# Kernel optimization log

Hardware: AMD Instinct MI355X
Metric: run time of the kernel (lower is better)

The kernel has to match this reference:

```python
import jax, jax.numpy as jnp
import numpy as np

N = 50000      # nodes
E = 800000     # edges (avg degree 16)
D_IN = 32      # raw feature dim
D = 96         # hidden == out dim (residual requires equality)
L = 4          # number of GatedGCN layers
NC = 10        # n_classes
EPS = 1e-6


def _w(k, shape, fan_in):
    return jax.random.normal(k, shape, jnp.float32) / np.sqrt(fan_in).astype(np.float32)


def setup_inputs() -> dict:
    key = jax.random.key(0)
    ks = jax.random.split(key, 16)
    inp = {
        'h': jax.random.normal(ks[0], (N, D_IN), jnp.float32),
        'e': jax.random.normal(ks[1], (E, D_IN), jnp.float32),
        'src': jax.random.randint(ks[2], (E,), 0, N, jnp.int32),
        'dst': jax.random.randint(ks[3], (E,), 0, N, jnp.int32),
        'fp_w': _w(ks[4], (D_IN, D), D_IN), 'fp_b': jnp.zeros((D,), jnp.float32),
        'ep_w': _w(ks[5], (D_IN, D), D_IN), 'ep_b': jnp.zeros((D,), jnp.float32),
    }
    for i, name in enumerate(['A', 'B', 'C', 'D', 'E']):
        inp[name + '_w'] = _w(ks[6 + i], (L, D, D), D)
        inp[name + '_b'] = jnp.zeros((L, D), jnp.float32)
    inp['mlp0_w'] = _w(ks[11], (D, D // 2), D); inp['mlp0_b'] = jnp.zeros((D // 2,), jnp.float32)
    inp['mlp1_w'] = _w(ks[12], (D // 2, D // 4), D // 2); inp['mlp1_b'] = jnp.zeros((D // 4,), jnp.float32)
    inp['mlp2_w'] = _w(ks[13], (D // 4, NC), D // 4); inp['mlp2_b'] = jnp.zeros((NC,), jnp.float32)
    return inp


def reference(h, e, src, dst, fp_w, fp_b, ep_w, ep_b,
              A_w, A_b, B_w, B_b, C_w, C_b, D_w, D_b, E_w, E_b,
              mlp0_w, mlp0_b, mlp1_w, mlp1_b, mlp2_w, mlp2_b):
    # input projections
    h = h @ fp_w + fp_b                       # [N, D]
    e = e @ ep_w + ep_b                       # [E, D]

    def layer(carry, p):
        h, e = carry
        Aw, Ab, Bw, Bb, Cw, Cb, Dw, Db, Ew, Eb = p
        Ah = h @ Aw + Ab
        Bh = h @ Bw + Bb
        Ce = e @ Cw + Cb
        Dh = h @ Dw + Db
        Eh = h @ Ew + Eb
        # edge gate: e_ij = D h_i + E h_j + C e_ij  (u_add_v with u=src, v=dst)
        e_new = Dh[src] + Eh[dst] + Ce          # [E, D]
        sigma = jax.nn.sigmoid(e_new)           # [E, D]
        # gated aggregation to destination nodes
        num = jax.ops.segment_sum(Bh[src] * sigma, dst, num_segments=N)  # [N, D]
        den = jax.ops.segment_sum(sigma, dst, num_segments=N)            # [N, D]
        h_new = Ah + num / (den + EPS)
        # relu then residual (batch_norm=False, dropout eval no-op)
        return (h + jax.nn.relu(h_new), e + jax.nn.relu(e_new)), None

    (h, e), _ = jax.lax.scan(layer, (h, e),
                             (A_w, A_b, B_w, B_b, C_w, C_b, D_w, D_b, E_w, E_b))

    # MLPReadout (L=2 halvings) + sigmoid head
    y = jax.nn.relu(h @ mlp0_w + mlp0_b)
    y = jax.nn.relu(y @ mlp1_w + mlp1_b)
    y = y @ mlp2_w + mlp2_b
    return jax.nn.sigmoid(y)                    # [N, NC]
```

## Files before the change

### kernel.cpp

```cpp
#include <hip/hip_runtime.h>

#define NN 50000
#define NE 800000
#define DIN 32
#define DD 96
#define NL 4
#define NCLS 10
#define EPSF 1e-6f

typedef unsigned short u16;
typedef unsigned int u32;

typedef __bf16 bf16x8 __attribute__((ext_vector_type(8)));
typedef float f32x4 __attribute__((ext_vector_type(4)));

static __device__ __forceinline__ u16 f2bf(float f) {
    u32 x = __float_as_uint(f);
    x += 0x7FFFu + ((x >> 16) & 1u);
    return (u16)(x >> 16);
}
static __device__ __forceinline__ u32 pk2(float a, float b) {
    u32 r;
    asm("v_cvt_pk_bf16_f32 %0, %1, %2" : "=v"(r) : "v"(a), "v"(b));
    return r;
}
static __device__ __forceinline__ float unlo(u32 u) { return __uint_as_float(u << 16); }
static __device__ __forceinline__ float unhi(u32 u) { return __uint_as_float(u & 0xFFFF0000u); }
static __device__ __forceinline__ float frcp(float x) { return __builtin_amdgcn_rcpf(x); }

__global__ void k_zero4(int* __restrict__ p, long n4) {
    long i = (long)blockIdx.x * blockDim.x + threadIdx.x;
    if (i < n4) ((int4*)p)[i] = make_int4(0, 0, 0, 0);
}

__global__ void k_hist(const int* __restrict__ dst, int* __restrict__ counts) {
    int i = blockIdx.x * blockDim.x + threadIdx.x;
    if (i < NE) atomicAdd(&counts[dst[i]], 1);
}

__global__ __launch_bounds__(1024) void k_scan1(const int* __restrict__ counts,
                                                int* __restrict__ excl,
                                                int* __restrict__ bsum, int n) {
    __shared__ int wsum[16];
    const int tid = threadIdx.x, lane = tid & 63, wid = tid >> 6;
    const int i = blockIdx.x * 1024 + tid;
    int v = (i < n) ? counts[i] : 0;
    int x = v;
#pragma unroll
    for (int off = 1; off < 64; off <<= 1) {
        int t = __shfl_up(x, (unsigned)off, 64);
        if (lane >= off) x += t;
    }
    if (lane == 63) wsum[wid] = x;
    __syncthreads();
    if (tid < 16) {
        int s = wsum[tid];
#pragma unroll
        for (int off = 1; off < 16; off <<= 1) {
            int t = __shfl_up(s, (unsigned)off, 16);
            if (tid >= off) s += t;
        }
        wsum[tid] = s;
    }
    __syncthreads();
    const int wbase = wid ? wsum[wid - 1] : 0;
    if (i < n) excl[i] = wbase + x - v;
    if (tid == 1023) bsum[blockIdx.x] = wbase + x;
}

__global__ void k_scan2(int* __restrict__ bsum, int nb) {
    const int lane = threadIdx.x;
    int v = (lane < nb) ? bsum[lane] : 0;
    int x = v;
#pragma unroll
    for (int off = 1; off < 64; off <<= 1) {
        int t = __shfl_up(x, (unsigned)off, 64);
        if (lane >= off) x += t;
    }
    if (lane < nb) bsum[lane] = x - v;
}

__global__ void k_scan3(int* __restrict__ row_ptr, int* __restrict__ cursor,
                        const int* __restrict__ bsum, int n) {
    int i = blockIdx.x * blockDim.x + threadIdx.x;
    if (i < n) {
        int v = row_ptr[i] + bsum[i >> 10];
        row_ptr[i] = v;
        cursor[i] = v;
    }
    if (i == 0) row_ptr[n] = NE;
}

__global__ void k_scatter(const int* __restrict__ src, const int* __restrict__ dst,
                          int* __restrict__ cursor, int* __restrict__ eperm,
                          int* __restrict__ srcp) {
    int i = blockIdx.x * blockDim.x + threadIdx.x;
    if (i >= NE) return;
    int pos = atomicAdd(&cursor[dst[i]], 1);
    eperm[pos] = i;
    srcp[pos] = src[i];
}

__global__ void k_packAll(const float* __restrict__ A_w, const float* __restrict__ B_w,
                          const float* __restrict__ C_w, const float* __restrict__ D_w,
                          const float* __restrict__ E_w,
                          const float* __restrict__ fp_w, const float* __restrict__ ep_w,
                          const float* __restrict__ m0w,
                          u16* __restrict__ awf, u16* __restrict__ bwf, u16* __restrict__ cwf,
                          u16* __restrict__ dwf, u16* __restrict__ ewf,
                          u16* __restrict__ wfp, u16* __restrict__ wep,
                          float* __restrict__ w0p) {
    const int PER = NL * 6 * 3 * 64;
    int q = blockIdx.x * blockDim.x + threadIdx.x;
    if (q < 5 * PER) {
        int which = q / PER;
        int qq = q - which * PER;
        const float* W_all = which == 0 ? A_w : which == 1 ? B_w : which == 2 ? C_w
                           : which == 3 ? D_w : E_w;
        u16* wf = which == 0 ? awf : which == 1 ? bwf : which == 2 ? cwf
                : which == 3 ? dwf : ewf;
        int l = qq / (6 * 3 * 64);
        int rem = qq - l * (6 * 3 * 64);
        int tile = rem / (3 * 64);
        int rem2 = rem - tile * (3 * 64);
        int c = rem2 >> 6, ln = rem2 & 63;
        const float* W = W_all + (long)l * DD * DD;
        int n = tile * 16 + (ln & 15);
        int k0 = c * 32 + (ln >> 4) * 8;
        u16 wv[8];
#pragma unroll
        for (int j = 0; j < 8; ++j) {
            int kk = k0 + j;
            int kact = (kk % 6) * 16 + kk / 6;
            wv[j] = f2bf(W[kact * DD + n]);
        }
        *(uint4*)&wf[(long)qq * 8] = *(uint4*)wv;
    } else if (q < 5 * PER + 768) {
        int qq = q - 5 * PER;
        int which = qq / 384; qq -= which * 384;
        const float* W = which ? ep_w : fp_w;
        u16* wf = which ? wep : wfp;
        int ln = qq & 63;
        int n = (qq >> 6) * 16 + (ln & 15);
        int k0 = (ln >> 4) * 8;
        u16 wv[8];
#pragma unroll
        for (int j = 0; j < 8; ++j) wv[j] = f2bf(W[(k0 + j) * DD + n]);
        *(uint4*)&wf[qq * 8] = *(uint4*)wv;
    } else {
        int qq = q - 5 * PER - 768;
        if (qq < DD * 48) {
            int p = qq / 48, j = qq - p * 48;
            int jp = (p % 6) * 16 + p / 6;
            w0p[qq] = m0w[jp * 48 + j];
        }
    }
}

template <bool BFOUT, bool PERM, bool POUT>
__global__ __launch_bounds__(256) void k_proj_m(const float* __restrict__ X,
                                                const u16* __restrict__ wf,
                                                const float* __restrict__ B,
                                                void* __restrict__ Y,
                                                const int* __restrict__ eperm,
                                                int ntiles) {
    const int lane = threadIdx.x & 63;
    const int gw = (blockIdx.x * blockDim.x + threadIdx.x) >> 6;
    const int nw = (gridDim.x * blockDim.x) >> 6;
    const int lm = lane & 15, quad = lane >> 4;

    bf16x8 bfr[6];
    float bias[6];
#pragma unroll
    for (int t = 0; t < 6; ++t) {
        bfr[t] = *(const bf16x8*)&wf[(t * 64 + lane) * 8];
        bias[t] = B[t * 16 + lm];
    }

    for (int tile = gw; tile < ntiles; tile += nw) {
        const int row = tile * 16 + lm;
        const long srow = PERM ? (long)eperm[row] : (long)row;
        float4 x0 = *(const float4*)&X[srow * DIN + quad * 8];
        float4 x1 = *(const float4*)&X[srow * DIN + quad * 8 + 4];
        u32 ap[4] = {pk2(x0.x, x0.y), pk2(x0.z, x0.w), pk2(x1.x, x1.y), pk2(x1.z, x1.w)};
        bf16x8 af = *(bf16x8*)ap;
        f32x4 acc[6];
#pragma unroll
        for (int t = 0; t < 6; ++t) {
            acc[t] = (f32x4){bias[t], bias[t], bias[t], bias[t]};
            acc[t] = __builtin_amdgcn_mfma_f32_16x16x32_bf16(af, bfr[t], acc[t], 0, 0, 0);
        }
        const long rbase = (long)tile * 16 + quad * 4;
        if (POUT) {
#pragma unroll
            for (int r = 0; r < 4; ++r) {
                if (BFOUT) {
                    u16* p = (u16*)Y + (rbase + r) * DD + lm * 6;
                    *(u32*)p       = pk2(acc[0][r], acc[1][r]);
                    *(u32*)(p + 2) = pk2(acc[2][r], acc[3][r]);
                    *(u32*)(p + 4) = pk2(acc[4][r], acc[5][r]);
                } else {
                    float* p = (float*)Y + (rbase + r) * DD + lm * 6;
                    *(float2*)(p)     = make_float2(acc[0][r], acc[1][r]);
                    *(float2*)(p + 2) = make_float2(acc[2][r], acc[3][r]);
                    *(float2*)(p + 4) = make_float2(acc[4][r], acc[5][r]);
                }
            }
        } else {
#pragma unroll
            for (int t = 0; t < 6; ++t) {
                const int j = t * 16 + lm;
#pragma unroll
                for (int r = 0; r < 4; ++r) {
                    float v = acc[t][r];
                    if (BFOUT) ((u16*)Y)[(rbase + r) * DD + j] = f2bf(v);
                    else       ((float*)Y)[(rbase + r) * DD + j] = v;
                }
            }
        }
    }
}

__global__ __launch_bounds__(256) void k_gemm4m(const float* __restrict__ X,
                                                const u16* __restrict__ awf, const float* __restrict__ ab,
                                                const u16* __restrict__ bwf, const float* __restrict__ bb,
                                                const u16* __restrict__ dwf, const float* __restrict__ db,
                                                const u16* __restrict__ ewf, const float* __restrict__ eb,
                                                float* __restrict__ Y0, u16* __restrict__ Y1,
                                                u16* __restrict__ Y2, u16* __restrict__ Y3,
                                                int ntiles) {
    const int lane = threadIdx.x & 63;
    const int w = threadIdx.x >> 6;
    const int lm = lane & 15, quad = lane >> 4;
    const u16* wf = (w == 0) ? awf : (w == 1) ? bwf : (w == 2) ? dwf : ewf;
    const float* bp = (w == 0) ? ab : (w == 1) ? bb : (w == 2) ? db : eb;

    bf16x8 bfr[6][3];
    float bias[6];
#pragma unroll
    for (int t = 0; t < 6; ++t) {
#pragma unroll
        for (int c = 0; c < 3; ++c)
            bfr[t][c] = *(const bf16x8*)&wf[((t * 3 + c) * 64 + lane) * 8];
        bias[t] = bp[t * 16 + lm];
    }

    for (int tile = blockIdx.x; tile < ntiles; tile += gridDim.x) {
        const float* xr = X + (long)(tile * 16 + lm) * DD;
        bf16x8 a[3];
#pragma unroll
        for (int c = 0; c < 3; ++c) {
            float4 x0 = *(const float4*)&xr[c * 32 + quad * 8];
            float4 x1 = *(const float4*)&xr[c * 32 + quad * 8 + 4];
            u32 ap[4] = {pk2(x0.x, x0.y), pk2(x0.z, x0.w), pk2(x1.x, x1.y), pk2(x1.z, x1.w)};
            a[c] = *(bf16x8*)ap;
        }
        f32x4 acc[6];
#pragma unroll
        for (int t = 0; t < 6; ++t) {
            acc[t] = (f32x4){bias[t], bias[t], bias[t], bias[t]};
#pragma unroll
            for (int c = 0; c < 3; ++c)
                acc[t] = __builtin_amdgcn_mfma_f32_16x16x32_bf16(a[c], bfr[t][c], acc[t], 0, 0, 0);
        }
        const long rbase = (long)tile * 16 + quad * 4;
        if (w == 0) {
#pragma unroll
            for (int r = 0; r < 4; ++r) {
                float* p = Y0 + (rbase + r) * DD + lm * 6;
                *(float2*)(p)     = make_float2(acc[0][r], acc[1][r]);
                *(float2*)(p + 2) = make_float2(acc[2][r], acc[3][r]);
                *(float2*)(p + 4) = make_float2(acc[4][r], acc[5][r]);
            }
        } else {
            u16* Yp = (w == 1) ? Y1 : (w == 2) ? Y2 : Y3;
#pragma unroll
            for (int r = 0; r < 4; ++r) {
                u16* p = Yp + (rbase + r) * DD + lm * 6;
                *(u32*)p       = pk2(acc[0][r], acc[1][r]);
                *(u32*)(p + 2) = pk2(acc[2][r], acc[3][r]);
                *(u32*)(p + 4) = pk2(acc[4][r], acc[5][r]);
            }
        }
    }
}

__global__ __launch_bounds__(256) void k_node_edge_w(u16* ebuf,
                                                     const u16* __restrict__ cwf,
                                                     const float* __restrict__ Cb,
                                                     const u16* __restrict__ Dh,
                                                     const u16* __restrict__ Eh,
                                                     const u16* __restrict__ Bh,
                                                     const int* __restrict__ srcp,
                                                     const int* __restrict__ row_ptr,
                                                     const float* __restrict__ Ah,
                                                     float* __restrict__ hbuf) {
    const int lane = threadIdx.x & 63;
    const int gw = (blockIdx.x * blockDim.x + threadIdx.x) >> 6;
    const int nw = (gridDim.x * blockDim.x) >> 6;
    const int lm = lane & 15, quad = lane >> 4;

    bf16x8 bfrag[6][3];
    float cb[6];
#pragma unroll
    for (int t = 0; t < 6; ++t) {
#pragma unroll
        for (int c = 0; c < 3; ++c)
            bfrag[t][c] = *(const bf16x8*)&cwf[((t * 3 + c) * 64 + lane) * 8];
        cb[t] = Cb[t * 16 + lm];
    }

    for (int n = gw; n < NN; n += nw) {
        const int r0 = row_ptr[n], r1 = row_ptr[n + 1];
        float nacc[6] = {0.f, 0.f, 0.f, 0.f, 0.f, 0.f};
        float dacc[6] = {0.f, 0.f, 0.f, 0.f, 0.f, 0.f};

        if (r0 < r1) {
            float ehc[6];
            {
                const u16* ep = Eh + (long)n * DD + lm * 6;
                u32 e0 = *(const u32*)ep, e1 = *(const u32*)(ep + 2), e2 = *(const u32*)(ep + 4);
                ehc[0] = cb[0] + unlo(e0); ehc[1] = cb[1] + unhi(e0);
                ehc[2] = cb[2] + unlo(e1); ehc[3] = cb[3] + unhi(e1);
                ehc[4] = cb[4] + unlo(e2); ehc[5] = cb[5] + unhi(e2);
            }
            bf16x8 a[3];
            {
                const int rows = r1 - r0 < 16 ? r1 - r0 : 16;
                const long arow = r0 + (lm < rows ? lm : 0);
#pragma unroll
                for (int c = 0; c < 3; ++c)
                    a[c] = *(const bf16x8*)&ebuf[arow * DD + c * 32 + quad * 8];
            }
            int sr[4];
#pragma unroll
            for (int r = 0; r < 4; ++r) {
                const int rl = quad * 4 + r;
                sr[r] = (r0 + rl < r1) ? srcp[r0 + rl] : 0;
            }

            for (int chunk = r0; chunk < r1; chunk += 16) {
                const int rows = r1 - chunk < 16 ? r1 - chunk : 16;
                f32x4 acc[6];
#pragma unroll
                for (int t = 0; t < 6; ++t) {
                    acc[t] = (f32x4){ehc[t], ehc[t], ehc[t], ehc[t]};
#pragma unroll
                    for (int c = 0; c < 3; ++c)
                        acc[t] = __builtin_amdgcn_mfma_f32_16x16x32_bf16(a[c], bfrag[t][c], acc[t], 0, 0, 0);
                }
                const int nchunk = chunk + 16;
                int srn[4] = {0, 0, 0, 0};
                if (nchunk < r1) {
                    const int rows2 = r1 - nchunk < 16 ? r1 - nchunk : 16;
                    const long arow2 = nchunk + (lm < rows2 ? lm : 0);
#pragma unroll
                    for (int c = 0; c < 3; ++c)
                        a[c] = *(const bf16x8*)&ebuf[arow2 * DD + c * 32 + quad * 8];
#pragma unroll
                    for (int r = 0; r < 4; ++r) {
                        const int rl = quad * 4 + r;
                        if (nchunk + rl < r1) srn[r] = srcp[nchunk + rl];
                    }
                }
#pragma unroll
                for (int r = 0; r < 4; ++r) {
                    const int rl = quad * 4 + r;
                    if (rl < rows) {
                        const long s = sr[r];
                        const u16* dp = Dh + s * DD + lm * 6;
                        const u16* bp = Bh + s * DD + lm * 6;
                        u16* ep = ebuf + (long)(chunk + rl) * DD + lm * 6;
                        u32 d0 = *(const u32*)dp, d1 = *(const u32*)(dp + 2), d2 = *(const u32*)(dp + 4);
                        u32 b0 = *(const u32*)bp, b1 = *(const u32*)(bp + 2), b2 = *(const u32*)(bp + 4);
                        u32 o0 = *(const u32*)ep, o1 = *(const u32*)(ep + 2), o2 = *(const u32*)(ep + 4);
                        float dh[6] = {unlo(d0), unhi(d0), unlo(d1), unhi(d1), unlo(d2), unhi(d2)};
                        float bh[6] = {unlo(b0), unhi(b0), unlo(b1), unhi(b1), unlo(b2), unhi(b2)};
                        float od[6] = {unlo(o0), unhi(o0), unlo(o1), unhi(o1), unlo(o2), unhi(o2)};
                        float ov[6];
#pragma unroll
                        for (int t = 0; t < 6; ++t) {
                            float en = acc[t][r] + dh[t];
                            float sg = frcp(1.f + __expf(-en));
                            nacc[t] += bh[t] * sg;
                            dacc[t] += sg;
                            ov[t] = od[t] + fmaxf(en, 0.f);
                        }
                        *(u32*)ep       = pk2(ov[0], ov[1]);
                        *(u32*)(ep + 2) = pk2(ov[2], ov[3]);
                        *(u32*)(ep + 4) = pk2(ov[4], ov[5]);
                    }
                }
#pragma unroll
                for (int r = 0; r < 4; ++r) sr[r] = srn[r];
            }
        }
#pragma unroll
        for (int t = 0; t < 6; ++t) {
            float x = nacc[t], y = dacc[t];
            x += __shfl_xor(x, 16); y += __shfl_xor(y, 16);
            x += __shfl_xor(x, 32); y += __shfl_xor(y, 32);
            nacc[t] = x; dacc[t] = y;
        }
        if (quad == 0) {
            const float* ap = Ah + (long)n * DD + lm * 6;
            float* hp = hbuf + (long)n * DD + lm * 6;
            float val[6];
#pragma unroll
            for (int t = 0; t < 6; ++t)
                val[t] = fmaxf(ap[t] + nacc[t] * frcp(dacc[t] + EPSF), 0.f);
            float2 h0 = *(float2*)hp, h1 = *(float2*)(hp + 2), h2 = *(float2*)(hp + 4);
            *(float2*)(hp)     = make_float2(h0.x + val[0], h0.y + val[1]);
            *(float2*)(hp + 2) = make_float2(h1.x + val[2], h1.y + val[3]);
            *(float2*)(hp + 4) = make_float2(h2.x + val[4], h2.y + val[5]);
        }
    }
}

__global__ void k_mlp(const float* __restrict__ X, const float* __restrict__ W,
                      const float* __restrict__ B, float* __restrict__ Y,
                      int K, int Dout, int act, long total) {
    long idx = (long)blockIdx.x * blockDim.x + threadIdx.x;
    if (idx >= total) return;
    int row = (int)(idx / Dout);
    int j = (int)(idx - (long)row * Dout);
    const float* xr = X + (long)row * K;
    float acc = B[j];
    for (int k = 0; k < K; ++k) acc = fmaf(xr[k], W[k * Dout + j], acc);
    if (act == 1) acc = fmaxf(acc, 0.f);
    else if (act == 2) acc = frcp(1.f + __expf(-acc));
    Y[idx] = acc;
}

extern "C" void kernel_launch(void* const* d_in, const int* in_sizes, int n_in,
                              void* d_out, int out_size, void* d_ws, size_t ws_size,
                              hipStream_t stream) {
    const float* h_in = (const float*)d_in[0];
    const float* e_in = (const float*)d_in[1];
    const int* src = (const int*)d_in[2];
    const int* dst = (const int*)d_in[3];
    const float* fp_w = (const float*)d_in[4];
    const float* fp_b = (const float*)d_in[5];
    const float* ep_w = (const float*)d_in[6];
    const float* ep_b = (const float*)d_in[7];
    const float* A_w = (const float*)d_in[8];
    const float* A_b = (const float*)d_in[9];
    const float* B_w = (const float*)d_in[10];
    const float* B_b = (const float*)d_in[11];
    const float* C_w = (const float*)d_in[12];
    const float* C_b = (const float*)d_in[13];
    const float* D_w = (const float*)d_in[14];
    const float* D_b = (const float*)d_in[15];
    const float* E_w = (const float*)d_in[16];
    const float* E_b = (const float*)d_in[17];
    const float* mlp0_w = (const float*)d_in[18];
    const float* mlp0_b = (const float*)d_in[19];
    const float* mlp1_w = (const float*)d_in[20];
    const float* mlp1_b = (const float*)d_in[21];
    const float* mlp2_w = (const float*)d_in[22];
    const float* mlp2_b = (const float*)d_in[23];
    float* out = (float*)d_out;

    const size_t ND_ = (size_t)NN * DD;
    const size_t ED_ = (size_t)NE * DD;
    const size_t FRAG = (size_t)NL * 6 * 3 * 64 * 8;
    char* w = (char*)d_ws;
    float* hbuf = (float*)w; w += ND_ * 4;
    float* Ahb  = (float*)w; w += ND_ * 4;
    u16* Bhb = (u16*)w; w += ND_ * 2;
    u16* Dhb = (u16*)w; w += ND_ * 2;
    u16* Ehb = (u16*)w; w += ND_ * 2;
    u16* ebuf = (u16*)w; w += ED_ * 2;
    int* counts  = (int*)w; w += (size_t)NN * 4;
    int* cursor  = (int*)w; w += (size_t)NN * 4;
    int* row_ptr = (int*)w; w += (size_t)(NN + 1) * 4 + 12;
    int* bsum    = (int*)w; w += 256;
    int* eperm   = (int*)w; w += (size_t)NE * 4;
    int* srcp    = (int*)w; w += (size_t)NE * 4;
    u16* awf = (u16*)w; w += FRAG * 2;
    u16* bwf = (u16*)w; w += FRAG * 2;
    u16* cwf = (u16*)w; w += FRAG * 2;
    u16* dwf = (u16*)w; w += FRAG * 2;
    u16* ewf = (u16*)w; w += FRAG * 2;
    u16* wfp = (u16*)w; w += (size_t)6 * 64 * 8 * 2;
    u16* wep = (u16*)w; w += (size_t)6 * 64 * 8 * 2;
    float* w0p = (float*)w; w += (size_t)DD * 48 * 4;
    size_t need = (size_t)(w - (char*)d_ws);
    if (ws_size < need) return;

    k_zero4<<<(NN / 4 + 255) / 256, 256, 0, stream>>>(counts, NN / 4);
    k_hist<<<(NE + 255) / 256, 256, 0, stream>>>(dst, counts);
    const int nsb = (NN + 1023) / 1024;
    k_scan1<<<nsb, 1024, 0, stream>>>(counts, row_ptr, bsum, NN);
    k_scan2<<<1, 64, 0, stream>>>(bsum, nsb);
    k_scan3<<<(NN + 255) / 256, 256, 0, stream>>>(row_ptr, cursor, bsum, NN);
    k_scatter<<<(NE + 255) / 256, 256, 0, stream>>>(src, dst, cursor, eperm, srcp);

    const int packTot = 5 * (NL * 6 * 3 * 64) + 768 + DD * 48;
    k_packAll<<<(packTot + 255) / 256, 256, 0, stream>>>(A_w, B_w, C_w, D_w, E_w,
                                                         fp_w, ep_w, mlp0_w,
                                                         awf, bwf, cwf, dwf, ewf,
                                                         wfp, wep, w0p);

    k_proj_m<false, false, true><<<256, 256, 0, stream>>>(h_in, wfp, fp_b, hbuf, nullptr, NN / 16);
    k_proj_m<true, true, true><<<2048, 256, 0, stream>>>(e_in, wep, ep_b, ebuf, eperm, NE / 16);

    const size_t LFRAG = (size_t)6 * 3 * 64 * 8;
    for (int l = 0; l < NL; ++l) {
        const float* Ab = A_b + (size_t)l * DD;
        const float* Bb = B_b + (size_t)l * DD;
        const float* Cb = C_b + (size_t)l * DD;
        const float* Db = D_b + (size_t)l * DD;
        const float* Eb = E_b + (size_t)l * DD;

        k_gemm4m<<<1280, 256, 0, stream>>>(hbuf,
                                           awf + l * LFRAG, Ab, bwf + l * LFRAG, Bb,
                                           dwf + l * LFRAG, Db, ewf + l * LFRAG, Eb,
                                           Ahb, Bhb, Dhb, Ehb, NN / 16);
        k_node_edge_w<<<2560, 256, 0, stream>>>(ebuf, cwf + l * LFRAG, Cb, Dhb, Ehb, Bhb,
                                                srcp, row_ptr, Ahb, hbuf);
    }

    float* y1 = Ahb;
    float* y2 = Ahb + (size_t)NN * 48;
    long t0 = (long)NN * 48, t1 = (long)NN * 24, t2 = (long)NN * NCLS;
    k_mlp<<<(int)((t0 + 255) / 256), 256, 0, stream>>>(hbuf, w0p, mlp0_b, y1, DD, 48, 1, t0);
    k_mlp<<<(int)((t1 + 255) / 256), 256, 0, stream>>>(y1, mlp1_w, mlp1_b, y2, 48, 24, 1, t1);
    k_mlp<<<(int)((t2 + 255) / 256), 256, 0, stream>>>(y2, mlp2_w, mlp2_b, out, 24, NCLS, 2, t2);
}
```

Before: 1.222 ms.

## Interleave Dh and Bh per node and scatter edge projection output

The GEMM kernel now writes the D and B projections into one interleaved 192-wide buffer, so the edge kernel fetches both source-node rows with three 8-byte loads instead of six 4-byte loads from two separate arrays. The scatter kernel now records each edge's sorted position, so the edge input projection reads its rows contiguously and scatters its output rows, instead of gathering input rows through a permutation. This cuts the number of random gather streams in the per-layer edge kernel, at the cost of scattered writes in the one-time projection.

```diff
diff --git a/kernel.cpp b/kernel.cpp
--- a/kernel.cpp
+++ b/kernel.cpp
@@ -92,12 +92,12 @@
 }
 
 __global__ void k_scatter(const int* __restrict__ src, const int* __restrict__ dst,
-                          int* __restrict__ cursor, int* __restrict__ eperm,
+                          int* __restrict__ cursor, int* __restrict__ inv,
                           int* __restrict__ srcp) {
     int i = blockIdx.x * blockDim.x + threadIdx.x;
     if (i >= NE) return;
     int pos = atomicAdd(&cursor[dst[i]], 1);
-    eperm[pos] = i;
+    inv[i] = pos;
     srcp[pos] = src[i];
 }
 
@@ -157,12 +157,12 @@
     }
 }
 
-template <bool BFOUT, bool PERM, bool POUT>
+template <bool BFOUT, bool POUT, bool SCAT>
 __global__ __launch_bounds__(256) void k_proj_m(const float* __restrict__ X,
                                                 const u16* __restrict__ wf,
                                                 const float* __restrict__ B,
                                                 void* __restrict__ Y,
-                                                const int* __restrict__ eperm,
+                                                const int* __restrict__ rmap,
                                                 int ntiles) {
     const int lane = threadIdx.x & 63;
     const int gw = (blockIdx.x * blockDim.x + threadIdx.x) >> 6;
@@ -178,8 +178,7 @@
     }
 
     for (int tile = gw; tile < ntiles; tile += nw) {
-        const int row = tile * 16 + lm;
-        const long srow = PERM ? (long)eperm[row] : (long)row;
+        const long srow = (long)tile * 16 + lm;
         float4 x0 = *(const float4*)&X[srow * DIN + quad * 8];
         float4 x1 = *(const float4*)&X[srow * DIN + quad * 8 + 4];
         u32 ap[4] = {pk2(x0.x, x0.y), pk2(x0.z, x0.w), pk2(x1.x, x1.y), pk2(x1.z, x1.w)};
@@ -194,13 +193,14 @@
         if (POUT) {
 #pragma unroll
             for (int r = 0; r < 4; ++r) {
+                const long orow = SCAT ? (long)rmap[rbase + r] : rbase + r;
                 if (BFOUT) {
-                    u16* p = (u16*)Y + (rbase + r) * DD + lm * 6;
+                    u16* p = (u16*)Y + orow * DD + lm * 6;
                     *(u32*)p       = pk2(acc[0][r], acc[1][r]);
                     *(u32*)(p + 2) = pk2(acc[2][r], acc[3][r]);
                     *(u32*)(p + 4) = pk2(acc[4][r], acc[5][r]);
                 } else {
-                    float* p = (float*)Y + (rbase + r) * DD + lm * 6;
+                    float* p = (float*)Y + orow * DD + lm * 6;
                     *(float2*)(p)     = make_float2(acc[0][r], acc[1][r]);
                     *(float2*)(p + 2) = make_float2(acc[2][r], acc[3][r]);
                     *(float2*)(p + 4) = make_float2(acc[4][r], acc[5][r]);
@@ -226,8 +226,8 @@
                                                 const u16* __restrict__ bwf, const float* __restrict__ bb,
                                                 const u16* __restrict__ dwf, const float* __restrict__ db,
                                                 const u16* __restrict__ ewf, const float* __restrict__ eb,
-                                                float* __restrict__ Y0, u16* __restrict__ Y1,
-                                                u16* __restrict__ Y2, u16* __restrict__ Y3,
+                                                float* __restrict__ Y0, u16* __restrict__ DBh,
+                                                u16* __restrict__ Y3,
                                                 int ntiles) {
     const int lane = threadIdx.x & 63;
     const int w = threadIdx.x >> 6;
@@ -272,15 +272,23 @@
                 *(float2*)(p + 2) = make_float2(acc[2][r], acc[3][r]);
                 *(float2*)(p + 4) = make_float2(acc[4][r], acc[5][r]);
             }
-        } else {
-            u16* Yp = (w == 1) ? Y1 : (w == 2) ? Y2 : Y3;
+        } else if (w == 3) {
 #pragma unroll
             for (int r = 0; r < 4; ++r) {
-                u16* p = Yp + (rbase + r) * DD + lm * 6;
+                u16* p = Y3 + (rbase + r) * DD + lm * 6;
                 *(u32*)p       = pk2(acc[0][r], acc[1][r]);
                 *(u32*)(p + 2) = pk2(acc[2][r], acc[3][r]);
                 *(u32*)(p + 4) = pk2(acc[4][r], acc[5][r]);
             }
+        } else {
+            const int off = (w == 1) ? 6 : 0;
+#pragma unroll
+            for (int r = 0; r < 4; ++r) {
+                u16* p = DBh + (rbase + r) * 192 + lm * 12 + off;
+                *(u32*)p       = pk2(acc[0][r], acc[1][r]);
+                *(u32*)(p + 2) = pk2(acc[2][r], acc[3][r]);
+                *(u32*)(p + 4) = pk2(acc[4][r], acc[5][r]);
+            }
         }
     }
 }
@@ -288,9 +296,8 @@
 __global__ __launch_bounds__(256) void k_node_edge_w(u16* ebuf,
                                                      const u16* __restrict__ cwf,
                                                      const float* __restrict__ Cb,
-                                                     const u16* __restrict__ Dh,
+                                                     const u16* __restrict__ DBh,
                                                      const u16* __restrict__ Eh,
-                                                     const u16* __restrict__ Bh,
                                                      const int* __restrict__ srcp,
                                                      const int* __restrict__ row_ptr,
                                                      const float* __restrict__ Ah,
@@ -368,14 +375,14 @@
                     const int rl = quad * 4 + r;
                     if (rl < rows) {
                         const long s = sr[r];
-                        const u16* dp = Dh + s * DD + lm * 6;
-                        const u16* bp = Bh + s * DD + lm * 6;
+                        const u16* dbp = DBh + s * 192 + lm * 12;
                         u16* ep = ebuf + (long)(chunk + rl) * DD + lm * 6;
-                        u32 d0 = *(const u32*)dp, d1 = *(const u32*)(dp + 2), d2 = *(const u32*)(dp + 4);
-                        u32 b0 = *(const u32*)bp, b1 = *(const u32*)(bp + 2), b2 = *(const u32*)(bp + 4);
+                        uint2 q0 = *(const uint2*)dbp;
+                        uint2 q1 = *(const uint2*)(dbp + 4);
+                        uint2 q2 = *(const uint2*)(dbp + 8);
                         u32 o0 = *(const u32*)ep, o1 = *(const u32*)(ep + 2), o2 = *(const u32*)(ep + 4);
-                        float dh[6] = {unlo(d0), unhi(d0), unlo(d1), unhi(d1), unlo(d2), unhi(d2)};
-                        float bh[6] = {unlo(b0), unhi(b0), unlo(b1), unhi(b1), unlo(b2), unhi(b2)};
+                        float dh[6] = {unlo(q0.x), unhi(q0.x), unlo(q0.y), unhi(q0.y), unlo(q1.x), unhi(q1.x)};
+                        float bh[6] = {unlo(q1.y), unhi(q1.y), unlo(q2.x), unhi(q2.x), unlo(q2.y), unhi(q2.y)};
                         float od[6] = {unlo(o0), unhi(o0), unlo(o1), unhi(o1), unlo(o2), unhi(o2)};
                         float ov[6];
 #pragma unroll
@@ -467,15 +474,14 @@
     char* w = (char*)d_ws;
     float* hbuf = (float*)w; w += ND_ * 4;
     float* Ahb  = (float*)w; w += ND_ * 4;
-    u16* Bhb = (u16*)w; w += ND_ * 2;
-    u16* Dhb = (u16*)w; w += ND_ * 2;
-    u16* Ehb = (u16*)w; w += ND_ * 2;
+    u16* DBhb = (u16*)w; w += (size_t)NN * 192 * 2;
+    u16* Ehb  = (u16*)w; w += ND_ * 2;
     u16* ebuf = (u16*)w; w += ED_ * 2;
     int* counts  = (int*)w; w += (size_t)NN * 4;
     int* cursor  = (int*)w; w += (size_t)NN * 4;
     int* row_ptr = (int*)w; w += (size_t)(NN + 1) * 4 + 12;
     int* bsum    = (int*)w; w += 256;
-    int* eperm   = (int*)w; w += (size_t)NE * 4;
+    int* inv     = (int*)w; w += (size_t)NE * 4;
     int* srcp    = (int*)w; w += (size_t)NE * 4;
     u16* awf = (u16*)w; w += FRAG * 2;
     u16* bwf = (u16*)w; w += FRAG * 2;
@@ -494,7 +500,7 @@
     k_scan1<<<nsb, 1024, 0, stream>>>(counts, row_ptr, bsum, NN);
     k_scan2<<<1, 64, 0, stream>>>(bsum, nsb);
     k_scan3<<<(NN + 255) / 256, 256, 0, stream>>>(row_ptr, cursor, bsum, NN);
-    k_scatter<<<(NE + 255) / 256, 256, 0, stream>>>(src, dst, cursor, eperm, srcp);
+    k_scatter<<<(NE + 255) / 256, 256, 0, stream>>>(src, dst, cursor, inv, srcp);
 
     const int packTot = 5 * (NL * 6 * 3 * 64) + 768 + DD * 48;
     k_packAll<<<(packTot + 255) / 256, 256, 0, stream>>>(A_w, B_w, C_w, D_w, E_w,
@@ -502,8 +508,8 @@
                                                          awf, bwf, cwf, dwf, ewf,
                                                          wfp, wep, w0p);
 
-    k_proj_m<false, false, true><<<256, 256, 0, stream>>>(h_in, wfp, fp_b, hbuf, nullptr, NN / 16);
-    k_proj_m<true, true, true><<<2048, 256, 0, stream>>>(e_in, wep, ep_b, ebuf, eperm, NE / 16);
+    k_proj_m<false, true, false><<<256, 256, 0, stream>>>(h_in, wfp, fp_b, hbuf, nullptr, NN / 16);
+    k_proj_m<true, true, true><<<2048, 256, 0, stream>>>(e_in, wep, ep_b, ebuf, inv, NE / 16);
 
     const size_t LFRAG = (size_t)6 * 3 * 64 * 8;
     for (int l = 0; l < NL; ++l) {
@@ -516,8 +522,8 @@
         k_gemm4m<<<1280, 256, 0, stream>>>(hbuf,
                                            awf + l * LFRAG, Ab, bwf + l * LFRAG, Bb,
                                            dwf + l * LFRAG, Db, ewf + l * LFRAG, Eb,
-                                           Ahb, Bhb, Dhb, Ehb, NN / 16);
-        k_node_edge_w<<<2560, 256, 0, stream>>>(ebuf, cwf + l * LFRAG, Cb, Dhb, Ehb, Bhb,
+                                           Ahb, DBhb, Ehb, NN / 16);
+        k_node_edge_w<<<2560, 256, 0, stream>>>(ebuf, cwf + l * LFRAG, Cb, DBhb, Ehb,
                                                 srcp, row_ptr, Ahb, hbuf);
     }
 
```

New measurement: 1.170 ms. 4.2% less time.
